# Performance work log

Measured on AMD Instinct MI355X. Metric: run time of the kernel, lower is better.

The kernel has to match this reference:

```python
import jax, jax.numpy as jnp
import numpy as np

B, H, W, C = 2, 64, 64, 512
EPS = 1e-3  # keras BatchNormalization default epsilon


def _bn(x, g, b, m, v):
    # inference-mode batch norm over the last axis
    return (x - m) * jax.lax.rsqrt(v + EPS) * g + b


def setup_inputs() -> dict:
    key = jax.random.key(0)
    ks = jax.random.split(key, 12)
    C2 = C // 2

    def he(k, shape, fan_in):
        return jax.random.normal(k, shape, jnp.float32) * np.float32(np.sqrt(2.0 / fan_in))

    def bn_params(k, n):
        k1, k2, k3, k4 = jax.random.split(k, 4)
        g = 1.0 + 0.1 * jax.random.normal(k1, (n,), jnp.float32)
        b = 0.1 * jax.random.normal(k2, (n,), jnp.float32)
        m = 0.1 * jax.random.normal(k3, (n,), jnp.float32)
        v = jax.random.uniform(k4, (n,), jnp.float32, 0.5, 1.5)
        return g, b, m, v

    g1, b1, m1, v1 = bn_params(ks[1], 1)
    g2, b2, m2, v2 = bn_params(ks[2], C2)
    g3, b3, m3, v3 = bn_params(ks[3], C2)
    g4, b4, m4, v4 = bn_params(ks[4], 1)
    g5, b5, m5, v5 = bn_params(ks[5], C)

    return {
        "x": jax.random.normal(ks[0], (B, H, W, C), jnp.float32),
        # edge_aggregation_func: Dense(1) over the 4-neighbor axis
        "w_ea": he(ks[6], (4, 1), 4), "b_ea": jnp.zeros((1,), jnp.float32),
        "g1": g1, "b1": b1, "m1": m1, "v1": v1,
        # vertex_update_func: Dense(C//2) over 2C features
        "w_vu": he(ks[7], (2 * C, C2), 2 * C), "b_vu": jnp.zeros((C2,), jnp.float32),
        "g2": g2, "b2": b2, "m2": m2, "v2": v2,
        # edge_update_func: Dense(C//2) over 2C features
        "w_eu": he(ks[8], (2 * C, C2), 2 * C), "b_eu": jnp.zeros((C2,), jnp.float32),
        "g3": g3, "b3": b3, "m3": m3, "v3": v3,
        # update_edge_reduce_func: Dense(1) over the 4-neighbor axis
        "w_er": he(ks[9], (4, 1), 4), "b_er": jnp.zeros((1,), jnp.float32),
        "g4": g4, "b4": b4, "m4": m4, "v4": v4,
        # final 1x1 conv (no bias): [C + C//2, C]
        "w_fc": he(ks[10], (C + C2, C), C + C2),
        "g5": g5, "b5": b5, "m5": m5, "v5": v5,
    }


def reference(x, w_ea, b_ea, g1, b1, m1, v1,
              w_vu, b_vu, g2, b2, m2, v2,
              w_eu, b_eu, g3, b3, m3, v3,
              w_er, b_er, g4, b4, m4, v4,
              w_fc, g5, b5, m5, v5):
    # 4-neighbor cyclic-shift edges: [B,H,W,C,4] (H+1, H-1, W+1, W-1 rolls)
    neigh = jnp.stack([
        jnp.roll(x, 1, axis=1), jnp.roll(x, -1, axis=1),
        jnp.roll(x, 1, axis=2), jnp.roll(x, -1, axis=2)], axis=-1)
    edge = neigh * x[..., None]                                   # [B,H,W,C,4]

    # edge aggregation: Dense(1) over neighbor axis + BN(1) + ReLU
    agg = jax.nn.relu(_bn(jnp.einsum('bhwcn,no->bhwco', edge, w_ea) + b_ea,
                          g1, b1, m1, v1))[..., 0]                # [B,H,W,C]

    # vertex update: Dense(C/2) on concat([vertex, agg]) + BN + ReLU
    cat_v = jnp.concatenate([x, agg], axis=-1)                    # [B,H,W,2C]
    uv = jax.nn.relu(_bn(cat_v @ w_vu + b_vu, g2, b2, m2, v2))    # [B,H,W,C/2]

    # edge update: Dense(C/2) on concat([vertex x4, edge]) along channel
    vert4 = jnp.broadcast_to(x[..., None], edge.shape)            # [B,H,W,C,4]
    cat_e = jnp.concatenate([vert4, edge], axis=3)                # [B,H,W,2C,4]
    ue = jax.nn.relu(_bn(jnp.einsum('bhwcn,cd->bhwnd', cat_e, w_eu) + b_eu,
                         g3, b3, m3, v3))                          # [B,H,W,4,C/2]

    # reduce updated edges over neighbor axis: Dense(1) + BN(1) + ReLU
    ur = jax.nn.relu(_bn(jnp.einsum('bhwnd,no->bhwdo', ue, w_er) + b_er,
                         g4, b4, m4, v4))[..., 0]                 # [B,H,W,C/2]

    update_feature = uv * ur                                      # [B,H,W,C/2]

    # final aggregation: 1x1 conv (no bias) on concat([x, update]) + BN + ReLU
    out = jax.nn.relu(_bn(jnp.concatenate([x, update_feature], axis=-1) @ w_fc,
                          g5, b5, m5, v5))                         # [B,H,W,C]
    return out
```

## Files before the change

kernel.cpp:

```cpp
#include <hip/hip_runtime.h>
#include <stdint.h>


typedef __attribute__((ext_vector_type(8))) short bf16x8;
typedef __attribute__((ext_vector_type(4))) float f32x4;

#define EPS_BN 1e-3f

__device__ __forceinline__ short f2bf(float f) {
    union { float f; unsigned u; } cv;
    cv.f = f;
    unsigned r = cv.u + 0x7fffu + ((cv.u >> 16) & 1u);
    return (short)(r >> 16);
}
__device__ __forceinline__ float bf2f(short s) {
    union { unsigned u; float f; } cv;
    cv.u = ((unsigned)(unsigned short)s) << 16;
    return cv.f;
}


__device__ __forceinline__ void pack_one(const float* __restrict__ W, short* __restrict__ out,
                                         int K, int Ncol, int lb, int tid) {
    int i = lb * 256 + tid;
    int lane = i & 63, tile = i >> 6;
    int ktiles = K >> 5;
    int nt = tile / ktiles, kt = tile - nt * ktiles;
    int kbase = (kt << 5) + ((lane >> 4) << 3);
    int col = (nt << 4) + (lane & 15);
    bf16x8 v;
    #pragma unroll
    for (int j = 0; j < 8; ++j) v[j] = f2bf(W[(kbase + j) * Ncol + col]);
    ((bf16x8*)out)[(tile << 6) + lane] = v;
}

__global__ __launch_bounds__(256) void k_setup(
    const float* w_vu, const float* w_eu, const float* w_fc,
    short* BpVu, short* BpEu, short* BpFc,
    const float* w_ea, const float* b_ea,
    const float* g1, const float* b1, const float* m1, const float* v1,
    const float* b_vu,
    const float* g2, const float* b2, const float* m2, const float* v2,
    const float* b_eu,
    const float* g3, const float* b3, const float* m3, const float* v3,
    const float* w_er, const float* b_er,
    const float* g4, const float* b4, const float* m4, const float* v4,
    const float* g5, const float* b5, const float* m5, const float* v5,
    float* P)
{
    int b = blockIdx.x, t = threadIdx.x;
    if (b < 128)      { pack_one(w_vu, BpVu, 1024, 256, b, t); }
    else if (b < 256) { pack_one(w_eu, BpEu, 1024, 256, b - 128, t); }
    else if (b < 448) { pack_one(w_fc, BpFc,  768, 512, b - 256, t); }
    else {
        for (int u = t; u < 512; u += 256) {
            float a5 = g5[u] * rsqrtf(v5[u] + EPS_BN);
            P[1032 + u] = a5;
            P[1544 + u] = b5[u] - m5[u] * a5;
        }
        {
            float a2 = g2[t] * rsqrtf(v2[t] + EPS_BN);
            P[8 + t]   = a2;
            P[264 + t] = (b_vu[t] - m2[t]) * a2 + b2[t];
            float a3 = g3[t] * rsqrtf(v3[t] + EPS_BN);
            P[520 + t] = a3;
            P[776 + t] = (b_eu[t] - m3[t]) * a3 + b3[t];
        }
        if (t < 4) {
            P[2056 + t] = w_ea[t];
            P[2060 + t] = w_er[t];
        }
        if (t == 0) {
            float a1 = g1[0] * rsqrtf(v1[0] + EPS_BN);
            P[0] = a1;
            P[1] = (b_ea[0] - m1[0]) * a1 + b1[0];
            float a4 = g4[0] * rsqrtf(v4[0] + EPS_BN);
            P[2] = a4;
            P[3] = (b_er[0] - m4[0]) * a4 + b4[0];
        }
    }
}

__global__ __launch_bounds__(256) void k_cvt_agg(const float* __restrict__ x,
                                                 const float* __restrict__ P,
                                                 short* __restrict__ xb,
                                                 short* __restrict__ agg,
                                                 short* __restrict__ prodD,
                                                 short* __restrict__ prodR)
{
    int idx = blockIdx.x * 256 + threadIdx.x;
    int n = idx >> 6;
    int ci = idx & 63;
    int bh = n >> 6, h = bh & 63, w = n & 63;
    int bhb = bh & ~63;
    int rowU = ((bhb + ((h + 63) & 63)) << 6) + w;
    int rowD = ((bhb + ((h + 1) & 63)) << 6) + w;
    int rowL = (bh << 6) + ((w + 63) & 63);
    int rowR = (bh << 6) + ((w + 1) & 63);

    const f32x4* xv = (const f32x4*)x;
    int c4 = ci << 1;
    f32x4 vc[2], vU[2], vD[2], vL[2], vR[2];
    #pragma unroll
    for (int h2 = 0; h2 < 2; ++h2) {
        vc[h2] = xv[(n    << 7) + c4 + h2];
        vU[h2] = xv[(rowU << 7) + c4 + h2];
        vD[h2] = xv[(rowD << 7) + c4 + h2];
        vL[h2] = xv[(rowL << 7) + c4 + h2];
        vR[h2] = xv[(rowR << 7) + c4 + h2];
    }

    float w0 = P[2056], w1 = P[2057], w2 = P[2058], w3 = P[2059];
    float a1 = P[0], c1 = P[1];
    bf16x8 ob, xbv, pD, pR;
    #pragma unroll
    for (int h2 = 0; h2 < 2; ++h2) {
        #pragma unroll
        for (int j = 0; j < 4; ++j) {
            int e = h2 * 4 + j;
            float xc = vc[h2][j];
            float eU = xc * vU[h2][j], eD = xc * vD[h2][j];
            float eL = xc * vL[h2][j], eR = xc * vR[h2][j];
            float S = w0 * eU + w1 * eD + w2 * eL + w3 * eR;
            ob[e]  = f2bf(fmaxf(fmaf(a1, S, c1), 0.f));
            xbv[e] = f2bf(xc);
            pD[e] = f2bf(eD); pR[e] = f2bf(eR);
        }
    }
    int o = (n << 6) + ci;
    ((bf16x8*)agg)[o] = ob;
    ((bf16x8*)xb)[o] = xbv;
    ((bf16x8*)prodD)[o] = pD;
    ((bf16x8*)prodR)[o] = pR;
}

__global__ __launch_bounds__(256) void k_gemm_mid(
    const short* __restrict__ xb, const short* __restrict__ agg,
    const short* __restrict__ prodD, const short* __restrict__ prodR,
    const short* __restrict__ BpVu, const short* __restrict__ BpEu,
    const float* __restrict__ P,
    short* __restrict__ uvb, short* __restrict__ tvb,
    short* __restrict__ teDb, short* __restrict__ teRb)
{
    __shared__ __align__(16) short lds[2][64 * 64];
    int t = threadIdx.x, l = t & 63, w = t >> 6;
    int type = blockIdx.x >> 7, rs = blockIdx.x & 127;
    int r0 = rs << 6;

    const short* A0; const short* A1; int nchunk, ktbase;
    const bf16x8* Bp; short* Out;
    if (type == 0)      { A0 = xb;    A1 = agg;   nchunk = 16; Bp = (const bf16x8*)BpVu; ktbase = 0;  Out = uvb;  }
    else if (type == 1) { A0 = xb;    A1 = xb;    nchunk = 8;  Bp = (const bf16x8*)BpEu; ktbase = 0;  Out = tvb;  }
    else if (type == 2) { A0 = prodD; A1 = prodD; nchunk = 8;  Bp = (const bf16x8*)BpEu; ktbase = 16; Out = teDb; }
    else                { A0 = prodR; A1 = prodR; nchunk = 8;  Bp = (const bf16x8*)BpEu; ktbase = 16; Out = teRb; }

    int dr = t >> 3;
    int lcs = ((t & 7) ^ (dr & 7)) << 3;
    int sr0 = (r0 + dr) << 9, sr1 = (r0 + dr + 32) << 9;

    f32x4 acc[4][4];
    #pragma unroll
    for (int mi = 0; mi < 4; ++mi)
        #pragma unroll
        for (int nf = 0; nf < 4; ++nf) acc[mi][nf] = (f32x4){0.f, 0.f, 0.f, 0.f};

    bf16x8 g0 = *(const bf16x8*)(A0 + sr0 + lcs);
    bf16x8 g1 = *(const bf16x8*)(A0 + sr1 + lcs);

    int buf = 0;
    for (int kc = 0; kc < nchunk; ++kc) {
        ((bf16x8*)lds[buf])[t] = g0;
        ((bf16x8*)lds[buf])[256 + t] = g1;
        __syncthreads();
        if (kc + 1 < nchunk) {
            int kn = kc + 1;
            const short* S = (kn < 8) ? A0 : A1;
            int off = (kn & 7) << 6;
            g0 = *(const bf16x8*)(S + sr0 + off + lcs);
            g1 = *(const bf16x8*)(S + sr1 + off + lcs);
        }
        const short* Lb = lds[buf];
        #pragma unroll
        for (int kt = 0; kt < 2; ++kt) {
            bf16x8 af[4];
            #pragma unroll
            for (int mi = 0; mi < 4; ++mi) {
                int row = (mi << 4) + (l & 15);
                int lcolb = (kt << 6) + ((l >> 4) << 4);
                int addr = (row << 6) + ((lcolb ^ ((row & 7) << 4)) >> 1);
                af[mi] = *(const bf16x8*)(Lb + addr);
            }
            int kt32 = ktbase + (kc << 1) + kt;
            #pragma unroll
            for (int nf = 0; nf < 4; ++nf) {
                bf16x8 b = Bp[((((w << 2) + nf) << 5) + kt32) * 64 + l];
                #pragma unroll
                for (int mi = 0; mi < 4; ++mi)
                    acc[mi][nf] = __builtin_amdgcn_mfma_f32_16x16x32_bf16(af[mi], b, acc[mi][nf], 0, 0, 0);
            }
        }
        buf ^= 1;
    }

    #pragma unroll
    for (int nf = 0; nf < 4; ++nf) {
        int col = (w << 6) + (nf << 4) + (l & 15);
        float aa = P[8 + col], cc = P[264 + col];
        #pragma unroll
        for (int mi = 0; mi < 4; ++mi) {
            int rbase = r0 + (mi << 4) + ((l >> 4) << 2);
            #pragma unroll
            for (int j = 0; j < 4; ++j) {
                float v = acc[mi][nf][j];
                if (type == 0) v = fmaxf(fmaf(v, aa, cc), 0.f);
                Out[(rbase + j) * 256 + col] = f2bf(v);
            }
        }
    }
}

__global__ __launch_bounds__(256) void k_ur_upd(
    const short* __restrict__ tv, const short* __restrict__ teD,
    const short* __restrict__ teR, const short* __restrict__ uv,
    const float* __restrict__ P, short* __restrict__ upd)
{
    int idx = blockIdx.x * 256 + threadIdx.x;
    int n = idx >> 5, c8 = idx & 31;
    int bh = n >> 6, h = bh & 63, w = n & 63;
    int bhb = bh & ~63;
    int nUp = ((bhb + ((h + 63) & 63)) << 6) + w;
    int nLf = (bh << 6) + ((w + 63) & 63);

    const bf16x8* TV = (const bf16x8*)tv;
    const bf16x8* TD = (const bf16x8*)teD;
    const bf16x8* TR = (const bf16x8*)teR;
    const bf16x8* UV = (const bf16x8*)uv;
    bf16x8 vTv = TV[n * 32 + c8];
    bf16x8 vD  = TD[n * 32 + c8];
    bf16x8 vDu = TD[nUp * 32 + c8];
    bf16x8 vR  = TR[n * 32 + c8];
    bf16x8 vRl = TR[nLf * 32 + c8];
    bf16x8 vUv = UV[n * 32 + c8];

    float w0 = P[2060], w1 = P[2061], w2 = P[2062], w3 = P[2063];
    float a4 = P[2], c4 = P[3];
    f32x4 a3lo = *(const f32x4*)&P[520 + c8 * 8], a3hi = *(const f32x4*)&P[524 + c8 * 8];
    f32x4 c3lo = *(const f32x4*)&P[776 + c8 * 8], c3hi = *(const f32x4*)&P[780 + c8 * 8];

    bf16x8 o;
    #pragma unroll
    for (int j = 0; j < 8; ++j) {
        float a3 = (j < 4) ? a3lo[j & 3] : a3hi[j & 3];
        float c3 = (j < 4) ? c3lo[j & 3] : c3hi[j & 3];
        float tvv = bf2f(vTv[j]);
        float ueU = fmaxf(fmaf(a3, tvv + bf2f(vDu[j]), c3), 0.f);
        float ueD = fmaxf(fmaf(a3, tvv + bf2f(vD[j]),  c3), 0.f);
        float ueL = fmaxf(fmaf(a3, tvv + bf2f(vRl[j]), c3), 0.f);
        float ueR = fmaxf(fmaf(a3, tvv + bf2f(vR[j]),  c3), 0.f);
        float s = w0 * ueU + w1 * ueD + w2 * ueL + w3 * ueR;
        float ur = fmaxf(fmaf(a4, s, c4), 0.f);
        o[j] = f2bf(ur * bf2f(vUv[j]));
    }
    ((bf16x8*)upd)[n * 32 + c8] = o;
}

__global__ __launch_bounds__(256) void k_gemm_out(
    const short* __restrict__ xb, const short* __restrict__ upd,
    const short* __restrict__ BpFc, const float* __restrict__ P,
    float* __restrict__ out)
{
    __shared__ __align__(16) short lds[2][32 * 64];
    int t = threadIdx.x, l = t & 63, w = t >> 6;
    int rs = blockIdx.x >> 1, cg = blockIdx.x & 1;
    int r0 = rs << 5;
    const bf16x8* Bp = (const bf16x8*)BpFc;

    int dr = t >> 3;
    int lcs = ((t & 7) ^ (dr & 7)) << 3;

    f32x4 acc[2][4];
    #pragma unroll
    for (int mi = 0; mi < 2; ++mi)
        #pragma unroll
        for (int nf = 0; nf < 4; ++nf) acc[mi][nf] = (f32x4){0.f, 0.f, 0.f, 0.f};

    bf16x8 g0 = *(const bf16x8*)(xb + ((r0 + dr) << 9) + lcs);
    int buf = 0;
    for (int kc = 0; kc < 12; ++kc) {
        ((bf16x8*)lds[buf])[t] = g0;
        __syncthreads();
        if (kc + 1 < 12) {
            int kn = kc + 1;
            if (kn < 8) g0 = *(const bf16x8*)(xb  + ((r0 + dr) << 9) + (kn << 6) + lcs);
            else        g0 = *(const bf16x8*)(upd + ((r0 + dr) << 8) + ((kn - 8) << 6) + lcs);
        }
        const short* Lb = lds[buf];
        #pragma unroll
        for (int kt = 0; kt < 2; ++kt) {
            bf16x8 af[2];
            #pragma unroll
            for (int mi = 0; mi < 2; ++mi) {
                int row = (mi << 4) + (l & 15);
                int lcolb = (kt << 6) + ((l >> 4) << 4);
                int addr = (row << 6) + ((lcolb ^ ((row & 7) << 4)) >> 1);
                af[mi] = *(const bf16x8*)(Lb + addr);
            }
            #pragma unroll
            for (int nf = 0; nf < 4; ++nf) {
                int nt = (cg << 4) + (w << 2) + nf;
                bf16x8 b = Bp[(nt * 24 + (kc << 1) + kt) * 64 + l];
                #pragma unroll
                for (int mi = 0; mi < 2; ++mi)
                    acc[mi][nf] = __builtin_amdgcn_mfma_f32_16x16x32_bf16(af[mi], b, acc[mi][nf], 0, 0, 0);
            }
        }
        buf ^= 1;
    }

    #pragma unroll
    for (int nf = 0; nf < 4; ++nf) {
        int col = (cg << 8) + (w << 6) + (nf << 4) + (l & 15);
        float a5 = P[1032 + col], c5 = P[1544 + col];
        #pragma unroll
        for (int mi = 0; mi < 2; ++mi) {
            int rbase = r0 + (mi << 4) + ((l >> 4) << 2);
            #pragma unroll
            for (int j = 0; j < 4; ++j) {
                out[(rbase + j) * 512 + col] = fmaxf(fmaf(acc[mi][nf][j], a5, c5), 0.f);
            }
        }
    }
}

extern "C" void kernel_launch(void* const* d_in, const int* in_sizes, int n_in,
                              void* d_out, int out_size, void* d_ws, size_t ws_size,
                              hipStream_t stream)
{
    const float* x    = (const float*)d_in[0];
    const float* w_ea = (const float*)d_in[1];
    const float* b_ea = (const float*)d_in[2];
    const float* g1   = (const float*)d_in[3];
    const float* b1   = (const float*)d_in[4];
    const float* m1   = (const float*)d_in[5];
    const float* v1   = (const float*)d_in[6];
    const float* w_vu = (const float*)d_in[7];
    const float* b_vu = (const float*)d_in[8];
    const float* g2   = (const float*)d_in[9];
    const float* b2   = (const float*)d_in[10];
    const float* m2   = (const float*)d_in[11];
    const float* v2   = (const float*)d_in[12];
    const float* w_eu = (const float*)d_in[13];
    const float* b_eu = (const float*)d_in[14];
    const float* g3   = (const float*)d_in[15];
    const float* b3   = (const float*)d_in[16];
    const float* m3   = (const float*)d_in[17];
    const float* v3   = (const float*)d_in[18];
    const float* w_er = (const float*)d_in[19];
    const float* b_er = (const float*)d_in[20];
    const float* g4   = (const float*)d_in[21];
    const float* b4   = (const float*)d_in[22];
    const float* m4   = (const float*)d_in[23];
    const float* v4   = (const float*)d_in[24];
    const float* w_fc = (const float*)d_in[25];
    const float* g5   = (const float*)d_in[26];
    const float* b5   = (const float*)d_in[27];
    const float* m5   = (const float*)d_in[28];
    const float* v5   = (const float*)d_in[29];

    char* ws = (char*)d_ws;
    float* P = (float*)ws;
    size_t off = 16384;
    short* BpVu = (short*)(ws + off); off += (size_t)1024 * 256 * 2;
    short* BpEu = (short*)(ws + off); off += (size_t)1024 * 256 * 2;
    short* BpFc = (short*)(ws + off); off += (size_t)768 * 512 * 2;
    short* xbb  = (short*)(ws + off); off += (size_t)8192 * 512 * 2;
    short* aggb = (short*)(ws + off); off += (size_t)8192 * 512 * 2;
    short* prodD = (short*)(ws + off); off += (size_t)8192 * 512 * 2;
    short* prodR = (short*)(ws + off); off += (size_t)8192 * 512 * 2;
    short* uvb  = (short*)(ws + off); off += (size_t)8192 * 256 * 2;
    short* tvb  = (short*)(ws + off); off += (size_t)8192 * 256 * 2;
    short* teDb = (short*)(ws + off); off += (size_t)8192 * 256 * 2;
    short* teRb = (short*)(ws + off); off += (size_t)8192 * 256 * 2;
    short* updb = (short*)(ws + off); off += (size_t)8192 * 256 * 2;

    k_setup<<<449, 256, 0, stream>>>(w_vu, w_eu, w_fc, BpVu, BpEu, BpFc,
                                     w_ea, b_ea, g1, b1, m1, v1,
                                     b_vu, g2, b2, m2, v2,
                                     b_eu, g3, b3, m3, v3,
                                     w_er, b_er, g4, b4, m4, v4,
                                     g5, b5, m5, v5, P);
    k_cvt_agg<<<2048, 256, 0, stream>>>(x, P, xbb, aggb, prodD, prodR);
    k_gemm_mid<<<512, 256, 0, stream>>>(xbb, aggb, prodD, prodR, BpVu, BpEu, P,
                                        uvb, tvb, teDb, teRb);
    k_ur_upd<<<1024, 256, 0, stream>>>(tvb, teDb, teRb, uvb, P, updb);
    k_gemm_out<<<512, 256, 0, stream>>>(xbb, updb, BpFc, P, (float*)d_out);
}
```

Baseline: 75.95 us.

## Fuse setup into front kernel, fuse edge-reduce into output GEMM, shrink tiles

Merges weight packing and BN-parameter setup into the x-conversion/aggregation kernel as extra blocks, which recomputes the scalar BN params locally so it no longer depends on P. It also folds the edge-reduce/update step into the final GEMM, which builds the update tile in LDS instead of writing and re-reading an intermediate buffer. Both GEMMs move to smaller 32-row tiles with more blocks for better occupancy. Together these cut two kernel launches and one global round trip, at the cost of more LDS per block in the output GEMM and redundant update computation across its four column-quarter blocks.

```diff
diff --git a/kernel.cpp b/kernel.cpp
--- a/kernel.cpp
+++ b/kernel.cpp
@@ -34,61 +34,61 @@
     ((bf16x8*)out)[(tile << 6) + lane] = v;
 }
 
-__global__ __launch_bounds__(256) void k_setup(
-    const float* w_vu, const float* w_eu, const float* w_fc,
-    short* BpVu, short* BpEu, short* BpFc,
+__global__ __launch_bounds__(256) void k_front(
+    const float* __restrict__ x,
     const float* w_ea, const float* b_ea,
     const float* g1, const float* b1, const float* m1, const float* v1,
-    const float* b_vu,
-    const float* g2, const float* b2, const float* m2, const float* v2,
-    const float* b_eu,
-    const float* g3, const float* b3, const float* m3, const float* v3,
+    const float* w_vu, const float* w_eu, const float* w_fc,
+    const float* b_vu, const float* g2, const float* b2_, const float* m2, const float* v2,
+    const float* b_eu, const float* g3, const float* b3, const float* m3, const float* v3,
     const float* w_er, const float* b_er,
     const float* g4, const float* b4, const float* m4, const float* v4,
     const float* g5, const float* b5, const float* m5, const float* v5,
-    float* P)
+    short* __restrict__ xb, short* __restrict__ agg,
+    short* __restrict__ prodD, short* __restrict__ prodR,
+    short* BpVu, short* BpEu, short* BpFc, float* P)
 {
-    int b = blockIdx.x, t = threadIdx.x;
-    if (b < 128)      { pack_one(w_vu, BpVu, 1024, 256, b, t); }
-    else if (b < 256) { pack_one(w_eu, BpEu, 1024, 256, b - 128, t); }
-    else if (b < 448) { pack_one(w_fc, BpFc,  768, 512, b - 256, t); }
-    else {
-        for (int u = t; u < 512; u += 256) {
-            float a5 = g5[u] * rsqrtf(v5[u] + EPS_BN);
-            P[1032 + u] = a5;
-            P[1544 + u] = b5[u] - m5[u] * a5;
-        }
-        {
-            float a2 = g2[t] * rsqrtf(v2[t] + EPS_BN);
-            P[8 + t]   = a2;
-            P[264 + t] = (b_vu[t] - m2[t]) * a2 + b2[t];
-            float a3 = g3[t] * rsqrtf(v3[t] + EPS_BN);
-            P[520 + t] = a3;
-            P[776 + t] = (b_eu[t] - m3[t]) * a3 + b3[t];
-        }
-        if (t < 4) {
-            P[2056 + t] = w_ea[t];
-            P[2060 + t] = w_er[t];
-        }
-        if (t == 0) {
-            float a1 = g1[0] * rsqrtf(v1[0] + EPS_BN);
-            P[0] = a1;
-            P[1] = (b_ea[0] - m1[0]) * a1 + b1[0];
-            float a4 = g4[0] * rsqrtf(v4[0] + EPS_BN);
-            P[2] = a4;
-            P[3] = (b_er[0] - m4[0]) * a4 + b4[0];
-        }
-    }
-}
-
-__global__ __launch_bounds__(256) void k_cvt_agg(const float* __restrict__ x,
-                                                 const float* __restrict__ P,
-                                                 short* __restrict__ xb,
-                                                 short* __restrict__ agg,
-                                                 short* __restrict__ prodD,
-                                                 short* __restrict__ prodR)
-{
-    int idx = blockIdx.x * 256 + threadIdx.x;
+    int blk = blockIdx.x, t = threadIdx.x;
+    if (blk >= 2048) {
+        int b = blk - 2048;
+        if (b < 128)      { pack_one(w_vu, BpVu, 1024, 256, b, t); }
+        else if (b < 256) { pack_one(w_eu, BpEu, 1024, 256, b - 128, t); }
+        else if (b < 448) { pack_one(w_fc, BpFc,  768, 512, b - 256, t); }
+        else {
+            for (int u = t; u < 512; u += 256) {
+                float a5 = g5[u] * rsqrtf(v5[u] + EPS_BN);
+                P[1032 + u] = a5;
+                P[1544 + u] = b5[u] - m5[u] * a5;
+            }
+            {
+                float a2 = g2[t] * rsqrtf(v2[t] + EPS_BN);
+                P[8 + t]   = a2;
+                P[264 + t] = (b_vu[t] - m2[t]) * a2 + b2_[t];
+                float a3 = g3[t] * rsqrtf(v3[t] + EPS_BN);
+                P[520 + t] = a3;
+                P[776 + t] = (b_eu[t] - m3[t]) * a3 + b3[t];
+            }
+            if (t < 4) {
+                P[2056 + t] = w_ea[t];
+                P[2060 + t] = w_er[t];
+            }
+            if (t == 0) {
+                float a4 = g4[0] * rsqrtf(v4[0] + EPS_BN);
+                P[2] = a4;
+                P[3] = (b_er[0] - m4[0]) * a4 + b4[0];
+                float a1l = g1[0] * rsqrtf(v1[0] + EPS_BN);
+                P[0] = a1l;
+                P[1] = (b_ea[0] - m1[0]) * a1l + b1[0];
+            }
+        }
+        return;
+    }
+
+    float a1 = g1[0] * rsqrtf(v1[0] + EPS_BN);
+    float c1 = (b_ea[0] - m1[0]) * a1 + b1[0];
+    float w0 = w_ea[0], w1 = w_ea[1], w2 = w_ea[2], w3 = w_ea[3];
+
+    int idx = blk * 256 + t;
     int n = idx >> 6;
     int ci = idx & 63;
     int bh = n >> 6, h = bh & 63, w = n & 63;
@@ -110,8 +110,6 @@
         vR[h2] = xv[(rowR << 7) + c4 + h2];
     }
 
-    float w0 = P[2056], w1 = P[2057], w2 = P[2058], w3 = P[2059];
-    float a1 = P[0], c1 = P[1];
     bf16x8 ob, xbv, pD, pR;
     #pragma unroll
     for (int h2 = 0; h2 < 2; ++h2) {
@@ -142,10 +140,10 @@
     short* __restrict__ uvb, short* __restrict__ tvb,
     short* __restrict__ teDb, short* __restrict__ teRb)
 {
-    __shared__ __align__(16) short lds[2][64 * 64];
+    __shared__ __align__(16) short sA[2][32 * 64];
     int t = threadIdx.x, l = t & 63, w = t >> 6;
-    int type = blockIdx.x >> 7, rs = blockIdx.x & 127;
-    int r0 = rs << 6;
+    int type = blockIdx.x & 3, rs = blockIdx.x >> 2;
+    int r0 = rs << 5;
 
     const short* A0; const short* A1; int nchunk, ktbase;
     const bf16x8* Bp; short* Out;
@@ -156,145 +154,26 @@
 
     int dr = t >> 3;
     int lcs = ((t & 7) ^ (dr & 7)) << 3;
-    int sr0 = (r0 + dr) << 9, sr1 = (r0 + dr + 32) << 9;
-
-    f32x4 acc[4][4];
-    #pragma unroll
-    for (int mi = 0; mi < 4; ++mi)
+    int srow = (r0 + dr) << 9;
+
+    f32x4 acc[2][4];
+    #pragma unroll
+    for (int mi = 0; mi < 2; ++mi)
         #pragma unroll
         for (int nf = 0; nf < 4; ++nf) acc[mi][nf] = (f32x4){0.f, 0.f, 0.f, 0.f};
 
-    bf16x8 g0 = *(const bf16x8*)(A0 + sr0 + lcs);
-    bf16x8 g1 = *(const bf16x8*)(A0 + sr1 + lcs);
+    bf16x8 g0 = *(const bf16x8*)(A0 + srow + lcs);
 
     int buf = 0;
     for (int kc = 0; kc < nchunk; ++kc) {
-        ((bf16x8*)lds[buf])[t] = g0;
-        ((bf16x8*)lds[buf])[256 + t] = g1;
+        ((bf16x8*)sA[buf])[t] = g0;
         __syncthreads();
         if (kc + 1 < nchunk) {
             int kn = kc + 1;
             const short* S = (kn < 8) ? A0 : A1;
-            int off = (kn & 7) << 6;
-            g0 = *(const bf16x8*)(S + sr0 + off + lcs);
-            g1 = *(const bf16x8*)(S + sr1 + off + lcs);
-        }
-        const short* Lb = lds[buf];
-        #pragma unroll
-        for (int kt = 0; kt < 2; ++kt) {
-            bf16x8 af[4];
-            #pragma unroll
-            for (int mi = 0; mi < 4; ++mi) {
-                int row = (mi << 4) + (l & 15);
-                int lcolb = (kt << 6) + ((l >> 4) << 4);
-                int addr = (row << 6) + ((lcolb ^ ((row & 7) << 4)) >> 1);
-                af[mi] = *(const bf16x8*)(Lb + addr);
-            }
-            int kt32 = ktbase + (kc << 1) + kt;
-            #pragma unroll
-            for (int nf = 0; nf < 4; ++nf) {
-                bf16x8 b = Bp[((((w << 2) + nf) << 5) + kt32) * 64 + l];
-                #pragma unroll
-                for (int mi = 0; mi < 4; ++mi)
-                    acc[mi][nf] = __builtin_amdgcn_mfma_f32_16x16x32_bf16(af[mi], b, acc[mi][nf], 0, 0, 0);
-            }
-        }
-        buf ^= 1;
-    }
-
-    #pragma unroll
-    for (int nf = 0; nf < 4; ++nf) {
-        int col = (w << 6) + (nf << 4) + (l & 15);
-        float aa = P[8 + col], cc = P[264 + col];
-        #pragma unroll
-        for (int mi = 0; mi < 4; ++mi) {
-            int rbase = r0 + (mi << 4) + ((l >> 4) << 2);
-            #pragma unroll
-            for (int j = 0; j < 4; ++j) {
-                float v = acc[mi][nf][j];
-                if (type == 0) v = fmaxf(fmaf(v, aa, cc), 0.f);
-                Out[(rbase + j) * 256 + col] = f2bf(v);
-            }
-        }
-    }
-}
-
-__global__ __launch_bounds__(256) void k_ur_upd(
-    const short* __restrict__ tv, const short* __restrict__ teD,
-    const short* __restrict__ teR, const short* __restrict__ uv,
-    const float* __restrict__ P, short* __restrict__ upd)
-{
-    int idx = blockIdx.x * 256 + threadIdx.x;
-    int n = idx >> 5, c8 = idx & 31;
-    int bh = n >> 6, h = bh & 63, w = n & 63;
-    int bhb = bh & ~63;
-    int nUp = ((bhb + ((h + 63) & 63)) << 6) + w;
-    int nLf = (bh << 6) + ((w + 63) & 63);
-
-    const bf16x8* TV = (const bf16x8*)tv;
-    const bf16x8* TD = (const bf16x8*)teD;
-    const bf16x8* TR = (const bf16x8*)teR;
-    const bf16x8* UV = (const bf16x8*)uv;
-    bf16x8 vTv = TV[n * 32 + c8];
-    bf16x8 vD  = TD[n * 32 + c8];
-    bf16x8 vDu = TD[nUp * 32 + c8];
-    bf16x8 vR  = TR[n * 32 + c8];
-    bf16x8 vRl = TR[nLf * 32 + c8];
-    bf16x8 vUv = UV[n * 32 + c8];
-
-    float w0 = P[2060], w1 = P[2061], w2 = P[2062], w3 = P[2063];
-    float a4 = P[2], c4 = P[3];
-    f32x4 a3lo = *(const f32x4*)&P[520 + c8 * 8], a3hi = *(const f32x4*)&P[524 + c8 * 8];
-    f32x4 c3lo = *(const f32x4*)&P[776 + c8 * 8], c3hi = *(const f32x4*)&P[780 + c8 * 8];
-
-    bf16x8 o;
-    #pragma unroll
-    for (int j = 0; j < 8; ++j) {
-        float a3 = (j < 4) ? a3lo[j & 3] : a3hi[j & 3];
-        float c3 = (j < 4) ? c3lo[j & 3] : c3hi[j & 3];
-        float tvv = bf2f(vTv[j]);
-        float ueU = fmaxf(fmaf(a3, tvv + bf2f(vDu[j]), c3), 0.f);
-        float ueD = fmaxf(fmaf(a3, tvv + bf2f(vD[j]),  c3), 0.f);
-        float ueL = fmaxf(fmaf(a3, tvv + bf2f(vRl[j]), c3), 0.f);
-        float ueR = fmaxf(fmaf(a3, tvv + bf2f(vR[j]),  c3), 0.f);
-        float s = w0 * ueU + w1 * ueD + w2 * ueL + w3 * ueR;
-        float ur = fmaxf(fmaf(a4, s, c4), 0.f);
-        o[j] = f2bf(ur * bf2f(vUv[j]));
-    }
-    ((bf16x8*)upd)[n * 32 + c8] = o;
-}
-
-__global__ __launch_bounds__(256) void k_gemm_out(
-    const short* __restrict__ xb, const short* __restrict__ upd,
-    const short* __restrict__ BpFc, const float* __restrict__ P,
-    float* __restrict__ out)
-{
-    __shared__ __align__(16) short lds[2][32 * 64];
-    int t = threadIdx.x, l = t & 63, w = t >> 6;
-    int rs = blockIdx.x >> 1, cg = blockIdx.x & 1;
-    int r0 = rs << 5;
-    const bf16x8* Bp = (const bf16x8*)BpFc;
-
-    int dr = t >> 3;
-    int lcs = ((t & 7) ^ (dr & 7)) << 3;
-
-    f32x4 acc[2][4];
-    #pragma unroll
-    for (int mi = 0; mi < 2; ++mi)
-        #pragma unroll
-        for (int nf = 0; nf < 4; ++nf) acc[mi][nf] = (f32x4){0.f, 0.f, 0.f, 0.f};
-
-    bf16x8 g0 = *(const bf16x8*)(xb + ((r0 + dr) << 9) + lcs);
-    int buf = 0;
-    for (int kc = 0; kc < 12; ++kc) {
-        ((bf16x8*)lds[buf])[t] = g0;
-        __syncthreads();
-        if (kc + 1 < 12) {
-            int kn = kc + 1;
-            if (kn < 8) g0 = *(const bf16x8*)(xb  + ((r0 + dr) << 9) + (kn << 6) + lcs);
-            else        g0 = *(const bf16x8*)(upd + ((r0 + dr) << 8) + ((kn - 8) << 6) + lcs);
-        }
-        const short* Lb = lds[buf];
+            g0 = *(const bf16x8*)(S + srow + ((kn & 7) << 6) + lcs);
+        }
+        const short* Lb = sA[buf];
         #pragma unroll
         for (int kt = 0; kt < 2; ++kt) {
             bf16x8 af[2];
@@ -305,21 +184,134 @@
                 int addr = (row << 6) + ((lcolb ^ ((row & 7) << 4)) >> 1);
                 af[mi] = *(const bf16x8*)(Lb + addr);
             }
+            int kt32 = ktbase + (kc << 1) + kt;
             #pragma unroll
             for (int nf = 0; nf < 4; ++nf) {
-                int nt = (cg << 4) + (w << 2) + nf;
+                bf16x8 b = Bp[((((w << 2) + nf) << 5) + kt32) * 64 + l];
+                #pragma unroll
+                for (int mi = 0; mi < 2; ++mi)
+                    acc[mi][nf] = __builtin_amdgcn_mfma_f32_16x16x32_bf16(af[mi], b, acc[mi][nf], 0, 0, 0);
+            }
+        }
+        buf ^= 1;
+    }
+
+    #pragma unroll
+    for (int nf = 0; nf < 4; ++nf) {
+        int col = (w << 6) + (nf << 4) + (l & 15);
+        float aa = P[8 + col], cc = P[264 + col];
+        #pragma unroll
+        for (int mi = 0; mi < 2; ++mi) {
+            int rbase = r0 + (mi << 4) + ((l >> 4) << 2);
+            #pragma unroll
+            for (int j = 0; j < 4; ++j) {
+                float v = acc[mi][nf][j];
+                if (type == 0) v = fmaxf(fmaf(v, aa, cc), 0.f);
+                Out[(rbase + j) * 256 + col] = f2bf(v);
+            }
+        }
+    }
+}
+
+__global__ __launch_bounds__(256) void k_gemm_out(
+    const short* __restrict__ xb,
+    const short* __restrict__ tv, const short* __restrict__ teD,
+    const short* __restrict__ teR, const short* __restrict__ uv,
+    const short* __restrict__ BpFc, const float* __restrict__ P,
+    float* __restrict__ out)
+{
+    __shared__ __align__(16) short sA[2][32 * 64];
+    __shared__ __align__(16) short updL[4][32 * 64];
+    int t = threadIdx.x, l = t & 63, w = t >> 6;
+    int cq = blockIdx.x & 3, rs = blockIdx.x >> 2;
+    int r0 = rs << 5;
+    const bf16x8* Bp = (const bf16x8*)BpFc;
+
+    int dr = t >> 3;
+    int p8 = t & 7;
+    int lcs = (p8 ^ (dr & 7)) << 3;
+
+    {
+        int n = r0 + dr;
+        int bh = n >> 6, h = bh & 63, ww = n & 63;
+        int bhb = bh & ~63;
+        int nUp = ((bhb + ((h + 63) & 63)) << 6) + ww;
+        int nLf = (bh << 6) + ((ww + 63) & 63);
+        float w0 = P[2060], w1 = P[2061], w2 = P[2062], w3 = P[2063];
+        float a4 = P[2], c4 = P[3];
+        #pragma unroll
+        for (int q = 0; q < 4; ++q) {
+            int lc = (q << 6) + lcs;
+            bf16x8 vTv = *(const bf16x8*)(tv  + n   * 256 + lc);
+            bf16x8 vD  = *(const bf16x8*)(teD + n   * 256 + lc);
+            bf16x8 vDu = *(const bf16x8*)(teD + nUp * 256 + lc);
+            bf16x8 vR  = *(const bf16x8*)(teR + n   * 256 + lc);
+            bf16x8 vRl = *(const bf16x8*)(teR + nLf * 256 + lc);
+            bf16x8 vUv = *(const bf16x8*)(uv  + n   * 256 + lc);
+            f32x4 a3a = *(const f32x4*)&P[520 + lc], a3b = *(const f32x4*)&P[524 + lc];
+            f32x4 c3a = *(const f32x4*)&P[776 + lc], c3b = *(const f32x4*)&P[780 + lc];
+            bf16x8 o;
+            #pragma unroll
+            for (int j = 0; j < 8; ++j) {
+                float a3 = (j < 4) ? a3a[j & 3] : a3b[j & 3];
+                float c3 = (j < 4) ? c3a[j & 3] : c3b[j & 3];
+                float tvv = bf2f(vTv[j]);
+                float ueU = fmaxf(fmaf(a3, tvv + bf2f(vDu[j]), c3), 0.f);
+                float ueD = fmaxf(fmaf(a3, tvv + bf2f(vD[j]),  c3), 0.f);
+                float ueL = fmaxf(fmaf(a3, tvv + bf2f(vRl[j]), c3), 0.f);
+                float ueR = fmaxf(fmaf(a3, tvv + bf2f(vR[j]),  c3), 0.f);
+                float s = w0 * ueU + w1 * ueD + w2 * ueL + w3 * ueR;
+                float ur = fmaxf(fmaf(a4, s, c4), 0.f);
+                o[j] = f2bf(ur * bf2f(vUv[j]));
+            }
+            *(bf16x8*)&updL[q][(dr << 6) + (p8 << 3)] = o;
+        }
+    }
+
+    f32x4 acc[2][2];
+    #pragma unroll
+    for (int mi = 0; mi < 2; ++mi)
+        #pragma unroll
+        for (int nf = 0; nf < 2; ++nf) acc[mi][nf] = (f32x4){0.f, 0.f, 0.f, 0.f};
+
+    bf16x8 g0 = *(const bf16x8*)(xb + ((r0 + dr) << 9) + lcs);
+    int buf = 0;
+    for (int kc = 0; kc < 12; ++kc) {
+        const short* Lb;
+        if (kc < 8) {
+            ((bf16x8*)sA[buf])[t] = g0;
+            __syncthreads();
+            if (kc + 1 < 8)
+                g0 = *(const bf16x8*)(xb + ((r0 + dr) << 9) + ((kc + 1) << 6) + lcs);
+            Lb = sA[buf];
+            buf ^= 1;
+        } else {
+            Lb = updL[kc - 8];
+        }
+        #pragma unroll
+        for (int kt = 0; kt < 2; ++kt) {
+            bf16x8 af[2];
+            #pragma unroll
+            for (int mi = 0; mi < 2; ++mi) {
+                int row = (mi << 4) + (l & 15);
+                int lcolb = (kt << 6) + ((l >> 4) << 4);
+                int addr = (row << 6) + ((lcolb ^ ((row & 7) << 4)) >> 1);
+                af[mi] = *(const bf16x8*)(Lb + addr);
+            }
+            #pragma unroll
+            for (int nf = 0; nf < 2; ++nf) {
+                int nt = (cq << 3) + (w << 1) + nf;
                 bf16x8 b = Bp[(nt * 24 + (kc << 1) + kt) * 64 + l];
                 #pragma unroll
                 for (int mi = 0; mi < 2; ++mi)
                     acc[mi][nf] = __builtin_amdgcn_mfma_f32_16x16x32_bf16(af[mi], b, acc[mi][nf], 0, 0, 0);
             }
         }
-        buf ^= 1;
-    }
-
-    #pragma unroll
-    for (int nf = 0; nf < 4; ++nf) {
-        int col = (cg << 8) + (w << 6) + (nf << 4) + (l & 15);
+    }
+
+    #pragma unroll
+    for (int nf = 0; nf < 2; ++nf) {
+        int col = (cq << 7) + (w << 5) + (nf << 4) + (l & 15);
         float a5 = P[1032 + col], c5 = P[1544 + col];
         #pragma unroll
         for (int mi = 0; mi < 2; ++mi) {
@@ -381,17 +373,17 @@
     short* tvb  = (short*)(ws + off); off += (size_t)8192 * 256 * 2;
     short* teDb = (short*)(ws + off); off += (size_t)8192 * 256 * 2;
     short* teRb = (short*)(ws + off); off += (size_t)8192 * 256 * 2;
-    short* updb = (short*)(ws + off); off += (size_t)8192 * 256 * 2;
-
-    k_setup<<<449, 256, 0, stream>>>(w_vu, w_eu, w_fc, BpVu, BpEu, BpFc,
-                                     w_ea, b_ea, g1, b1, m1, v1,
-                                     b_vu, g2, b2, m2, v2,
-                                     b_eu, g3, b3, m3, v3,
-                                     w_er, b_er, g4, b4, m4, v4,
-                                     g5, b5, m5, v5, P);
-    k_cvt_agg<<<2048, 256, 0, stream>>>(x, P, xbb, aggb, prodD, prodR);
-    k_gemm_mid<<<512, 256, 0, stream>>>(xbb, aggb, prodD, prodR, BpVu, BpEu, P,
-                                        uvb, tvb, teDb, teRb);
-    k_ur_upd<<<1024, 256, 0, stream>>>(tvb, teDb, teRb, uvb, P, updb);
-    k_gemm_out<<<512, 256, 0, stream>>>(xbb, updb, BpFc, P, (float*)d_out);
-}
+
+    k_front<<<2497, 256, 0, stream>>>(x, w_ea, b_ea, g1, b1, m1, v1,
+                                      w_vu, w_eu, w_fc,
+                                      b_vu, g2, b2, m2, v2,
+                                      b_eu, g3, b3, m3, v3,
+                                      w_er, b_er, g4, b4, m4, v4,
+                                      g5, b5, m5, v5,
+                                      xbb, aggb, prodD, prodR,
+                                      BpVu, BpEu, BpFc, P);
+    k_gemm_mid<<<1024, 256, 0, stream>>>(xbb, aggb, prodD, prodR, BpVu, BpEu, P,
+                                         uvb, tvb, teDb, teRb);
+    k_gemm_out<<<1024, 256, 0, stream>>>(xbb, tvb, teDb, teRb, uvb, BpFc, P,
+                                         (float*)d_out);
+}
```

Measured after the change: 69.68 us. 1.09x faster.

## Merge setup into front kernel and drop LDS staging in GEMMs

Applied to the files above, without the earlier changes.

The weight-packing/BN-parameter setup kernel is folded into the conversion/aggregation kernel as extra blocks, removing one launch; the aggregation path now computes its BN constants inline instead of reading them from P. Both GEMM kernels drop LDS double-buffering and load MFMA A-fragments directly from global memory, with smaller 32-row tiles in the mid GEMM (doubling its grid) and launch bounds asking for 4 blocks per CU. This removes syncthreads and LDS traffic and raises occupancy, but A fragments are now fetched with less coalesced per-lane loads and there is no explicit prefetch, so latency hiding depends on occupancy.

```diff
diff --git a/kernel.cpp b/kernel.cpp
--- a/kernel.cpp
+++ b/kernel.cpp
@@ -6,6 +6,7 @@
 typedef __attribute__((ext_vector_type(4))) float f32x4;
 
 #define EPS_BN 1e-3f
+#define MFMA16(a, b, c) __builtin_amdgcn_mfma_f32_16x16x32_bf16(a, b, c, 0, 0, 0)
 
 __device__ __forceinline__ short f2bf(float f) {
     union { float f; unsigned u; } cv;
@@ -34,61 +35,61 @@
     ((bf16x8*)out)[(tile << 6) + lane] = v;
 }
 
-__global__ __launch_bounds__(256) void k_setup(
-    const float* w_vu, const float* w_eu, const float* w_fc,
-    short* BpVu, short* BpEu, short* BpFc,
+__global__ __launch_bounds__(256) void k_front(
+    const float* __restrict__ x,
     const float* w_ea, const float* b_ea,
     const float* g1, const float* b1, const float* m1, const float* v1,
-    const float* b_vu,
-    const float* g2, const float* b2, const float* m2, const float* v2,
-    const float* b_eu,
-    const float* g3, const float* b3, const float* m3, const float* v3,
+    const float* w_vu, const float* w_eu, const float* w_fc,
+    const float* b_vu, const float* g2, const float* b2_, const float* m2, const float* v2,
+    const float* b_eu, const float* g3, const float* b3, const float* m3, const float* v3,
     const float* w_er, const float* b_er,
     const float* g4, const float* b4, const float* m4, const float* v4,
     const float* g5, const float* b5, const float* m5, const float* v5,
-    float* P)
-{
-    int b = blockIdx.x, t = threadIdx.x;
-    if (b < 128)      { pack_one(w_vu, BpVu, 1024, 256, b, t); }
-    else if (b < 256) { pack_one(w_eu, BpEu, 1024, 256, b - 128, t); }
-    else if (b < 448) { pack_one(w_fc, BpFc,  768, 512, b - 256, t); }
-    else {
-        for (int u = t; u < 512; u += 256) {
-            float a5 = g5[u] * rsqrtf(v5[u] + EPS_BN);
-            P[1032 + u] = a5;
-            P[1544 + u] = b5[u] - m5[u] * a5;
-        }
-        {
-            float a2 = g2[t] * rsqrtf(v2[t] + EPS_BN);
-            P[8 + t]   = a2;
-            P[264 + t] = (b_vu[t] - m2[t]) * a2 + b2[t];
-            float a3 = g3[t] * rsqrtf(v3[t] + EPS_BN);
-            P[520 + t] = a3;
-            P[776 + t] = (b_eu[t] - m3[t]) * a3 + b3[t];
-        }
-        if (t < 4) {
-            P[2056 + t] = w_ea[t];
-            P[2060 + t] = w_er[t];
-        }
-        if (t == 0) {
-            float a1 = g1[0] * rsqrtf(v1[0] + EPS_BN);
-            P[0] = a1;
-            P[1] = (b_ea[0] - m1[0]) * a1 + b1[0];
-            float a4 = g4[0] * rsqrtf(v4[0] + EPS_BN);
-            P[2] = a4;
-            P[3] = (b_er[0] - m4[0]) * a4 + b4[0];
-        }
-    }
-}
-
-__global__ __launch_bounds__(256) void k_cvt_agg(const float* __restrict__ x,
-                                                 const float* __restrict__ P,
-                                                 short* __restrict__ xb,
-                                                 short* __restrict__ agg,
-                                                 short* __restrict__ prodD,
-                                                 short* __restrict__ prodR)
-{
-    int idx = blockIdx.x * 256 + threadIdx.x;
+    short* __restrict__ xb, short* __restrict__ agg,
+    short* __restrict__ prodD, short* __restrict__ prodR,
+    short* BpVu, short* BpEu, short* BpFc, float* P)
+{
+    int blk = blockIdx.x, t = threadIdx.x;
+    if (blk >= 2048) {
+        int b = blk - 2048;
+        if (b < 128)      { pack_one(w_vu, BpVu, 1024, 256, b, t); }
+        else if (b < 256) { pack_one(w_eu, BpEu, 1024, 256, b - 128, t); }
+        else if (b < 448) { pack_one(w_fc, BpFc,  768, 512, b - 256, t); }
+        else {
+            for (int u = t; u < 512; u += 256) {
+                float a5 = g5[u] * rsqrtf(v5[u] + EPS_BN);
+                P[1032 + u] = a5;
+                P[1544 + u] = b5[u] - m5[u] * a5;
+            }
+            {
+                float a2 = g2[t] * rsqrtf(v2[t] + EPS_BN);
+                P[8 + t]   = a2;
+                P[264 + t] = (b_vu[t] - m2[t]) * a2 + b2_[t];
+                float a3 = g3[t] * rsqrtf(v3[t] + EPS_BN);
+                P[520 + t] = a3;
+                P[776 + t] = (b_eu[t] - m3[t]) * a3 + b3[t];
+            }
+            if (t < 4) {
+                P[2056 + t] = w_ea[t];
+                P[2060 + t] = w_er[t];
+            }
+            if (t == 0) {
+                float a4 = g4[0] * rsqrtf(v4[0] + EPS_BN);
+                P[2] = a4;
+                P[3] = (b_er[0] - m4[0]) * a4 + b4[0];
+                float a1l = g1[0] * rsqrtf(v1[0] + EPS_BN);
+                P[0] = a1l;
+                P[1] = (b_ea[0] - m1[0]) * a1l + b1[0];
+            }
+        }
+        return;
+    }
+
+    float a1 = g1[0] * rsqrtf(v1[0] + EPS_BN);
+    float c1 = (b_ea[0] - m1[0]) * a1 + b1[0];
+    float w0 = w_ea[0], w1 = w_ea[1], w2 = w_ea[2], w3 = w_ea[3];
+
+    int idx = blk * 256 + t;
     int n = idx >> 6;
     int ci = idx & 63;
     int bh = n >> 6, h = bh & 63, w = n & 63;
@@ -110,8 +111,6 @@
         vR[h2] = xv[(rowR << 7) + c4 + h2];
     }
 
-    float w0 = P[2056], w1 = P[2057], w2 = P[2058], w3 = P[2059];
-    float a1 = P[0], c1 = P[1];
     bf16x8 ob, xbv, pD, pR;
     #pragma unroll
     for (int h2 = 0; h2 < 2; ++h2) {
@@ -124,7 +123,8 @@
             float S = w0 * eU + w1 * eD + w2 * eL + w3 * eR;
             ob[e]  = f2bf(fmaxf(fmaf(a1, S, c1), 0.f));
             xbv[e] = f2bf(xc);
-            pD[e] = f2bf(eD); pR[e] = f2bf(eR);
+            pD[e] = f2bf(eD);
+            pR[e] = f2bf(eR);
         }
     }
     int o = (n << 6) + ci;
@@ -134,7 +134,7 @@
     ((bf16x8*)prodR)[o] = pR;
 }
 
-__global__ __launch_bounds__(256) void k_gemm_mid(
+__global__ __launch_bounds__(256, 4) void k_gemm_mid(
     const short* __restrict__ xb, const short* __restrict__ agg,
     const short* __restrict__ prodD, const short* __restrict__ prodR,
     const short* __restrict__ BpVu, const short* __restrict__ BpEu,
@@ -142,64 +142,52 @@
     short* __restrict__ uvb, short* __restrict__ tvb,
     short* __restrict__ teDb, short* __restrict__ teRb)
 {
-    __shared__ __align__(16) short lds[2][64 * 64];
     int t = threadIdx.x, l = t & 63, w = t >> 6;
-    int type = blockIdx.x >> 7, rs = blockIdx.x & 127;
-    int r0 = rs << 6;
-
-    const short* A0; const short* A1; int nchunk, ktbase;
-    const bf16x8* Bp; short* Out;
-    if (type == 0)      { A0 = xb;    A1 = agg;   nchunk = 16; Bp = (const bf16x8*)BpVu; ktbase = 0;  Out = uvb;  }
-    else if (type == 1) { A0 = xb;    A1 = xb;    nchunk = 8;  Bp = (const bf16x8*)BpEu; ktbase = 0;  Out = tvb;  }
-    else if (type == 2) { A0 = prodD; A1 = prodD; nchunk = 8;  Bp = (const bf16x8*)BpEu; ktbase = 16; Out = teDb; }
-    else                { A0 = prodR; A1 = prodR; nchunk = 8;  Bp = (const bf16x8*)BpEu; ktbase = 16; Out = teRb; }
-
-    int dr = t >> 3;
-    int lcs = ((t & 7) ^ (dr & 7)) << 3;
-    int sr0 = (r0 + dr) << 9, sr1 = (r0 + dr + 32) << 9;
-
-    f32x4 acc[4][4];
-    #pragma unroll
-    for (int mi = 0; mi < 4; ++mi)
+    int type = blockIdx.x >> 8, rs = blockIdx.x & 255;
+    int r0 = rs << 5;
+    int arow0 = (r0 + (l & 15)) << 9;
+    int arow1 = (r0 + 16 + (l & 15)) << 9;
+    int kseg = (l >> 4) << 3;
+    int nt0 = w << 2;
+
+    const short* Asrc = (type == 1) ? xb : (type == 2) ? prodD : prodR;
+    const bf16x8* Bp = (type == 0) ? (const bf16x8*)BpVu : (const bf16x8*)BpEu;
+    int ktbase = (type >= 2) ? 16 : 0;
+    short* Out = (type == 0) ? uvb : (type == 1) ? tvb : (type == 2) ? teDb : teRb;
+
+    f32x4 acc[2][4];
+    #pragma unroll
+    for (int mi = 0; mi < 2; ++mi)
         #pragma unroll
         for (int nf = 0; nf < 4; ++nf) acc[mi][nf] = (f32x4){0.f, 0.f, 0.f, 0.f};
 
-    bf16x8 g0 = *(const bf16x8*)(A0 + sr0 + lcs);
-    bf16x8 g1 = *(const bf16x8*)(A0 + sr1 + lcs);
-
-    int buf = 0;
-    for (int kc = 0; kc < nchunk; ++kc) {
-        ((bf16x8*)lds[buf])[t] = g0;
-        ((bf16x8*)lds[buf])[256 + t] = g1;
-        __syncthreads();
-        if (kc + 1 < nchunk) {
-            int kn = kc + 1;
-            const short* S = (kn < 8) ? A0 : A1;
-            int off = (kn & 7) << 6;
-            g0 = *(const bf16x8*)(S + sr0 + off + lcs);
-            g1 = *(const bf16x8*)(S + sr1 + off + lcs);
-        }
-        const short* Lb = lds[buf];
-        #pragma unroll
-        for (int kt = 0; kt < 2; ++kt) {
-            bf16x8 af[4];
-            #pragma unroll
-            for (int mi = 0; mi < 4; ++mi) {
-                int row = (mi << 4) + (l & 15);
-                int lcolb = (kt << 6) + ((l >> 4) << 4);
-                int addr = (row << 6) + ((lcolb ^ ((row & 7) << 4)) >> 1);
-                af[mi] = *(const bf16x8*)(Lb + addr);
-            }
-            int kt32 = ktbase + (kc << 1) + kt;
+    if (type == 0) {
+        #pragma unroll 4
+        for (int kt = 0; kt < 32; ++kt) {
+            const short* S = (kt < 16) ? xb : agg;
+            int ko = ((kt & 15) << 5) + kseg;
+            bf16x8 a0 = *(const bf16x8*)(S + arow0 + ko);
+            bf16x8 a1 = *(const bf16x8*)(S + arow1 + ko);
             #pragma unroll
             for (int nf = 0; nf < 4; ++nf) {
-                bf16x8 b = Bp[((((w << 2) + nf) << 5) + kt32) * 64 + l];
-                #pragma unroll
-                for (int mi = 0; mi < 4; ++mi)
-                    acc[mi][nf] = __builtin_amdgcn_mfma_f32_16x16x32_bf16(af[mi], b, acc[mi][nf], 0, 0, 0);
-            }
-        }
-        buf ^= 1;
+                bf16x8 b = Bp[(((nt0 + nf) << 5) + kt) * 64 + l];
+                acc[0][nf] = MFMA16(a0, b, acc[0][nf]);
+                acc[1][nf] = MFMA16(a1, b, acc[1][nf]);
+            }
+        }
+    } else {
+        #pragma unroll 4
+        for (int kt = 0; kt < 16; ++kt) {
+            int ko = (kt << 5) + kseg;
+            bf16x8 a0 = *(const bf16x8*)(Asrc + arow0 + ko);
+            bf16x8 a1 = *(const bf16x8*)(Asrc + arow1 + ko);
+            #pragma unroll
+            for (int nf = 0; nf < 4; ++nf) {
+                bf16x8 b = Bp[(((nt0 + nf) << 5) + ktbase + kt) * 64 + l];
+                acc[0][nf] = MFMA16(a0, b, acc[0][nf]);
+                acc[1][nf] = MFMA16(a1, b, acc[1][nf]);
+            }
+        }
     }
 
     #pragma unroll
@@ -207,7 +195,7 @@
         int col = (w << 6) + (nf << 4) + (l & 15);
         float aa = P[8 + col], cc = P[264 + col];
         #pragma unroll
-        for (int mi = 0; mi < 4; ++mi) {
+        for (int mi = 0; mi < 2; ++mi) {
             int rbase = r0 + (mi << 4) + ((l >> 4) << 2);
             #pragma unroll
             for (int j = 0; j < 4; ++j) {
@@ -264,62 +252,54 @@
     ((bf16x8*)upd)[n * 32 + c8] = o;
 }
 
-__global__ __launch_bounds__(256) void k_gemm_out(
+__global__ __launch_bounds__(256, 4) void k_gemm_out(
     const short* __restrict__ xb, const short* __restrict__ upd,
     const short* __restrict__ BpFc, const float* __restrict__ P,
     float* __restrict__ out)
 {
-    __shared__ __align__(16) short lds[2][32 * 64];
     int t = threadIdx.x, l = t & 63, w = t >> 6;
-    int rs = blockIdx.x >> 1, cg = blockIdx.x & 1;
+    int ch = blockIdx.x & 1, rs = blockIdx.x >> 1;
     int r0 = rs << 5;
+    int xr0 = (r0 + (l & 15)) << 9, xr1 = (r0 + 16 + (l & 15)) << 9;
+    int ur0 = (r0 + (l & 15)) << 8, ur1 = (r0 + 16 + (l & 15)) << 8;
+    int kseg = (l >> 4) << 3;
+    int nt0 = (ch << 4) + (w << 2);
     const bf16x8* Bp = (const bf16x8*)BpFc;
 
-    int dr = t >> 3;
-    int lcs = ((t & 7) ^ (dr & 7)) << 3;
-
     f32x4 acc[2][4];
     #pragma unroll
     for (int mi = 0; mi < 2; ++mi)
         #pragma unroll
         for (int nf = 0; nf < 4; ++nf) acc[mi][nf] = (f32x4){0.f, 0.f, 0.f, 0.f};
 
-    bf16x8 g0 = *(const bf16x8*)(xb + ((r0 + dr) << 9) + lcs);
-    int buf = 0;
-    for (int kc = 0; kc < 12; ++kc) {
-        ((bf16x8*)lds[buf])[t] = g0;
-        __syncthreads();
-        if (kc + 1 < 12) {
-            int kn = kc + 1;
-            if (kn < 8) g0 = *(const bf16x8*)(xb  + ((r0 + dr) << 9) + (kn << 6) + lcs);
-            else        g0 = *(const bf16x8*)(upd + ((r0 + dr) << 8) + ((kn - 8) << 6) + lcs);
-        }
-        const short* Lb = lds[buf];
-        #pragma unroll
-        for (int kt = 0; kt < 2; ++kt) {
-            bf16x8 af[2];
-            #pragma unroll
-            for (int mi = 0; mi < 2; ++mi) {
-                int row = (mi << 4) + (l & 15);
-                int lcolb = (kt << 6) + ((l >> 4) << 4);
-                int addr = (row << 6) + ((lcolb ^ ((row & 7) << 4)) >> 1);
-                af[mi] = *(const bf16x8*)(Lb + addr);
-            }
-            #pragma unroll
-            for (int nf = 0; nf < 4; ++nf) {
-                int nt = (cg << 4) + (w << 2) + nf;
-                bf16x8 b = Bp[(nt * 24 + (kc << 1) + kt) * 64 + l];
-                #pragma unroll
-                for (int mi = 0; mi < 2; ++mi)
-                    acc[mi][nf] = __builtin_amdgcn_mfma_f32_16x16x32_bf16(af[mi], b, acc[mi][nf], 0, 0, 0);
-            }
-        }
-        buf ^= 1;
+    #pragma unroll 4
+    for (int kt = 0; kt < 16; ++kt) {
+        int ko = (kt << 5) + kseg;
+        bf16x8 a0 = *(const bf16x8*)(xb + xr0 + ko);
+        bf16x8 a1 = *(const bf16x8*)(xb + xr1 + ko);
+        #pragma unroll
+        for (int nf = 0; nf < 4; ++nf) {
+            bf16x8 b = Bp[((nt0 + nf) * 24 + kt) * 64 + l];
+            acc[0][nf] = MFMA16(a0, b, acc[0][nf]);
+            acc[1][nf] = MFMA16(a1, b, acc[1][nf]);
+        }
+    }
+    #pragma unroll 4
+    for (int kt = 0; kt < 8; ++kt) {
+        int ko = (kt << 5) + kseg;
+        bf16x8 a0 = *(const bf16x8*)(upd + ur0 + ko);
+        bf16x8 a1 = *(const bf16x8*)(upd + ur1 + ko);
+        #pragma unroll
+        for (int nf = 0; nf < 4; ++nf) {
+            bf16x8 b = Bp[((nt0 + nf) * 24 + 16 + kt) * 64 + l];
+            acc[0][nf] = MFMA16(a0, b, acc[0][nf]);
+            acc[1][nf] = MFMA16(a1, b, acc[1][nf]);
+        }
     }
 
     #pragma unroll
     for (int nf = 0; nf < 4; ++nf) {
-        int col = (cg << 8) + (w << 6) + (nf << 4) + (l & 15);
+        int col = (ch << 8) + (w << 6) + (nf << 4) + (l & 15);
         float a5 = P[1032 + col], c5 = P[1544 + col];
         #pragma unroll
         for (int mi = 0; mi < 2; ++mi) {
@@ -383,15 +363,17 @@
     short* teRb = (short*)(ws + off); off += (size_t)8192 * 256 * 2;
     short* updb = (short*)(ws + off); off += (size_t)8192 * 256 * 2;
 
-    k_setup<<<449, 256, 0, stream>>>(w_vu, w_eu, w_fc, BpVu, BpEu, BpFc,
-                                     w_ea, b_ea, g1, b1, m1, v1,
-                                     b_vu, g2, b2, m2, v2,
-                                     b_eu, g3, b3, m3, v3,
-                                     w_er, b_er, g4, b4, m4, v4,
-                                     g5, b5, m5, v5, P);
-    k_cvt_agg<<<2048, 256, 0, stream>>>(x, P, xbb, aggb, prodD, prodR);
-    k_gemm_mid<<<512, 256, 0, stream>>>(xbb, aggb, prodD, prodR, BpVu, BpEu, P,
-                                        uvb, tvb, teDb, teRb);
+    k_front<<<2497, 256, 0, stream>>>(x, w_ea, b_ea, g1, b1, m1, v1,
+                                      w_vu, w_eu, w_fc,
+                                      b_vu, g2, b2, m2, v2,
+                                      b_eu, g3, b3, m3, v3,
+                                      w_er, b_er, g4, b4, m4, v4,
+                                      g5, b5, m5, v5,
+                                      xbb, aggb, prodD, prodR,
+                                      BpVu, BpEu, BpFc, P);
+    k_gemm_mid<<<1024, 256, 0, stream>>>(xbb, aggb, prodD, prodR,
+                                         BpVu, BpEu, P,
+                                         uvb, tvb, teDb, teRb);
     k_ur_upd<<<1024, 256, 0, stream>>>(tvb, teDb, teRb, uvb, P, updb);
     k_gemm_out<<<512, 256, 0, stream>>>(xbb, updb, BpFc, P, (float*)d_out);
 }
```

After: 84.79 us. 1.12x slower.
